# Kernel optimization log

Measured on AMD Instinct MI355X. Metric: run time of the kernel, lower is better.

Reference implementation:

```python
import jax, jax.numpy as jnp
import numpy as np

VARIANCE = 1.0  # prototorch euclidean_similarity default


def setup_inputs() -> dict:
    key = jax.random.key(0)
    k1, k2, k3 = jax.random.split(key, 3)
    B, D = 32768, 1024
    K, C = 5, 3  # sum([2,1,2]) components, len([2,1,2]) classes
    x = jax.random.normal(k1, (B, D), dtype=jnp.float32)
    components = jax.random.normal(k2, (K, D), dtype=jnp.float32)
    # PPRI: random probabilistic reasonings in [0,1], shape [K, C, 2]
    reasonings = jax.random.uniform(k3, (K, C, 2), dtype=jnp.float32)
    return {"x": x, "components": components, "reasonings": reasonings}


def reference(x, components, reasonings):
    # --- euclidean similarity: exp(-d(x, c)^2 / (2*variance)) ---
    # squared pairwise distances via expansion (avoids [B,K,D] intermediate)
    x2 = jnp.sum(x * x, axis=-1, keepdims=True)          # [B,1]
    c2 = jnp.sum(components * components, axis=-1)       # [K]
    d2 = x2 + c2[None, :] - 2.0 * (x @ components.T)     # [B,K]
    d2 = jnp.maximum(d2, 0.0)
    sims = jnp.exp(-d2 / (2.0 * VARIANCE))               # [B,K]

    # --- cbcc competition ---
    # reasonings [K,C,2] -> permute(2,1,0) -> [2,C,K], clamp to [0,1]
    R = jnp.clip(jnp.transpose(reasonings, (2, 1, 0)), 0.0, 1.0)
    A, Bneg = R[0], R[1]                                 # each [C,K]
    pk = A
    nk = (1.0 - A) * Bneg                                # [C,K]
    numerator = sims @ (pk - nk).T + jnp.sum(nk, axis=1) # [B,C]
    probs = numerator / jnp.sum(pk + nk, axis=1)         # [B,C]
    return probs
```

## Files before the change

### kernel.cpp

```cpp
#include <hip/hip_runtime.h>


#define DD 1024
#define KK 5
#define CC 3
#define F4_PER_ROW (DD / 4)
#define F4_PER_LANE (F4_PER_ROW / 64)

__global__ __launch_bounds__(256) void cbc_kernel(
    const float* __restrict__ x,
    const float* __restrict__ comps,
    const float* __restrict__ reas,
    float* __restrict__ out,
    int B)
{
    const int lane = threadIdx.x & 63;
    const int waves_per_block = blockDim.x >> 6;
    const int wave_global = blockIdx.x * waves_per_block + (threadIdx.x >> 6);
    const int n_waves = gridDim.x * waves_per_block;

    float4 cf[KK][F4_PER_LANE];
    const float4* comps4 = (const float4*)comps;
#pragma unroll
    for (int k = 0; k < KK; ++k)
#pragma unroll
        for (int j = 0; j < F4_PER_LANE; ++j)
            cf[k][j] = comps4[k * F4_PER_ROW + j * 64 + lane];

    float w[CC][KK], bias[CC], invden[CC];
#pragma unroll
    for (int c = 0; c < CC; ++c) {
        float nsum = 0.f, dsum = 0.f;
#pragma unroll
        for (int k = 0; k < KK; ++k) {
            float a = reas[k * (CC * 2) + c * 2 + 0];
            float b = reas[k * (CC * 2) + c * 2 + 1];
            a = fminf(fmaxf(a, 0.f), 1.f);
            b = fminf(fmaxf(b, 0.f), 1.f);
            float nk = (1.f - a) * b;
            w[c][k] = a - nk;
            nsum += nk;
            dsum += a + nk;
        }
        bias[c] = nsum;
        invden[c] = 1.f / dsum;
    }

    const float4* x4 = (const float4*)x;

    for (int row = wave_global; row < B; row += n_waves) {
        float acc[KK];
#pragma unroll
        for (int k = 0; k < KK; ++k) acc[k] = 0.f;

#pragma unroll
        for (int j = 0; j < F4_PER_LANE; ++j) {
            float4 xv = x4[(size_t)row * F4_PER_ROW + j * 64 + lane];
#pragma unroll
            for (int k = 0; k < KK; ++k) {
                float dx = xv.x - cf[k][j].x;
                float dy = xv.y - cf[k][j].y;
                float dz = xv.z - cf[k][j].z;
                float dw = xv.w - cf[k][j].w;
                acc[k] += dx * dx;
                acc[k] += dy * dy;
                acc[k] += dz * dz;
                acc[k] += dw * dw;
            }
        }

#pragma unroll
        for (int k = 0; k < KK; ++k) {
#pragma unroll
            for (int off = 32; off > 0; off >>= 1)
                acc[k] += __shfl_xor(acc[k], off, 64);
        }

        float sims[KK];
#pragma unroll
        for (int k = 0; k < KK; ++k)
            sims[k] = __expf(-0.5f * acc[k]);

        if (lane < CC) {
            const int c = lane;
            float num = bias[c];
#pragma unroll
            for (int k = 0; k < KK; ++k) num += sims[k] * w[c][k];
            out[(size_t)row * CC + c] = num * invden[c];
        }
    }
}

extern "C" void kernel_launch(void* const* d_in, const int* in_sizes, int n_in,
                              void* d_out, int out_size, void* d_ws, size_t ws_size,
                              hipStream_t stream) {
    const float* x = (const float*)d_in[0];
    const float* comps = (const float*)d_in[1];
    const float* reas = (const float*)d_in[2];
    float* out = (float*)d_out;
    const int B = in_sizes[0] / DD;

    const int blocks = 1024;
    cbc_kernel<<<blocks, 256, 0, stream>>>(x, comps, reas, out, B);
}
```

Measured before the change: 191.0 us.

## Prefetch next row into registers and use dot-product distance expansion

Each wave now loads the next row's data into registers while computing the current row, so memory latency overlaps with compute. Squared distances are computed as x²+c²−2x·c, with the component norms precomputed once per wave, which removes the per-element subtractions. The grid is doubled to raise the number of waves in flight. The costs are higher register pressure and slightly different floating-point rounding from the expansion.

```diff
diff --git a/kernel.cpp b/kernel.cpp
--- a/kernel.cpp
+++ b/kernel.cpp
@@ -27,6 +27,23 @@
         for (int j = 0; j < F4_PER_LANE; ++j)
             cf[k][j] = comps4[k * F4_PER_ROW + j * 64 + lane];
 
+    float c2[KK];
+#pragma unroll
+    for (int k = 0; k < KK; ++k) {
+        float s = 0.f;
+#pragma unroll
+        for (int j = 0; j < F4_PER_LANE; ++j) {
+            s += cf[k][j].x * cf[k][j].x;
+            s += cf[k][j].y * cf[k][j].y;
+            s += cf[k][j].z * cf[k][j].z;
+            s += cf[k][j].w * cf[k][j].w;
+        }
+#pragma unroll
+        for (int off = 32; off > 0; off >>= 1)
+            s += __shfl_xor(s, off, 64);
+        c2[k] = s;
+    }
+
     float w[CC][KK], bias[CC], invden[CC];
 #pragma unroll
     for (int c = 0; c < CC; ++c) {
@@ -48,38 +65,54 @@
 
     const float4* x4 = (const float4*)x;
 
-    for (int row = wave_global; row < B; row += n_waves) {
-        float acc[KK];
+    int row = wave_global;
+    if (row >= B) return;
+
+    float4 xv[F4_PER_LANE];
 #pragma unroll
-        for (int k = 0; k < KK; ++k) acc[k] = 0.f;
+    for (int j = 0; j < F4_PER_LANE; ++j)
+        xv[j] = x4[(size_t)row * F4_PER_ROW + j * 64 + lane];
 
+    for (; row < B; row += n_waves) {
+        const int nrow = (row + n_waves < B) ? (row + n_waves) : row;
+        float4 nx[F4_PER_LANE];
+#pragma unroll
+        for (int j = 0; j < F4_PER_LANE; ++j)
+            nx[j] = x4[(size_t)nrow * F4_PER_ROW + j * 64 + lane];
+
+        float dot[KK];
+        float x2 = 0.f;
+#pragma unroll
+        for (int k = 0; k < KK; ++k) dot[k] = 0.f;
 #pragma unroll
         for (int j = 0; j < F4_PER_LANE; ++j) {
-            float4 xv = x4[(size_t)row * F4_PER_ROW + j * 64 + lane];
+            const float4 v = xv[j];
+            x2 += v.x * v.x + v.y * v.y + v.z * v.z + v.w * v.w;
 #pragma unroll
             for (int k = 0; k < KK; ++k) {
-                float dx = xv.x - cf[k][j].x;
-                float dy = xv.y - cf[k][j].y;
-                float dz = xv.z - cf[k][j].z;
-                float dw = xv.w - cf[k][j].w;
-                acc[k] += dx * dx;
-                acc[k] += dy * dy;
-                acc[k] += dz * dz;
-                acc[k] += dw * dw;
+                dot[k] += v.x * cf[k][j].x;
+                dot[k] += v.y * cf[k][j].y;
+                dot[k] += v.z * cf[k][j].z;
+                dot[k] += v.w * cf[k][j].w;
             }
         }
 
 #pragma unroll
+        for (int off = 32; off > 0; off >>= 1)
+            x2 += __shfl_xor(x2, off, 64);
+#pragma unroll
         for (int k = 0; k < KK; ++k) {
 #pragma unroll
             for (int off = 32; off > 0; off >>= 1)
-                acc[k] += __shfl_xor(acc[k], off, 64);
+                dot[k] += __shfl_xor(dot[k], off, 64);
         }
 
         float sims[KK];
 #pragma unroll
-        for (int k = 0; k < KK; ++k)
-            sims[k] = __expf(-0.5f * acc[k]);
+        for (int k = 0; k < KK; ++k) {
+            float d2 = fmaxf(x2 + c2[k] - 2.f * dot[k], 0.f);
+            sims[k] = __expf(-0.5f * d2);
+        }
 
         if (lane < CC) {
             const int c = lane;
@@ -88,6 +121,9 @@
             for (int k = 0; k < KK; ++k) num += sims[k] * w[c][k];
             out[(size_t)row * CC + c] = num * invden[c];
         }
+
+#pragma unroll
+        for (int j = 0; j < F4_PER_LANE; ++j) xv[j] = nx[j];
     }
 }
 
@@ -100,6 +136,6 @@
     float* out = (float*)d_out;
     const int B = in_sizes[0] / DD;
 
-    const int blocks = 1024;
+    const int blocks = 2048;
     cbc_kernel<<<blocks, 256, 0, stream>>>(x, comps, reas, out, B);
 }
```

Result: no change. 194.8 us (+2.0%).
